# Kernel tuning notes

Hardware: AMD Instinct MI355X
Metric: run time of the kernel (lower is better)

Reference implementation:

```python
import jax, jax.numpy as jnp
import numpy as np

B = 32            # graphs in batch
NPG = 2048        # nodes per graph (equal-size graphs -> static topk sizes)
N = B * NPG
DEG = 8
E = N * DEG
IN = 64
H1 = 2 * IN       # 128
H2 = 2 * H1       # 256
K1 = NPG // 2     # SAGPooling ratio=0.5
K2 = K1 // 2
EPS = 1e-5


def _lin(k, fi, fo):
    s = 1.0 / np.sqrt(fi)
    return jax.random.uniform(k, (fi, fo), jnp.float32, -s, s)


def setup_inputs() -> dict:
    key = jax.random.key(0)
    ks = jax.random.split(key, 24)
    x = jax.random.normal(ks[0], (N, IN), jnp.float32)
    # edges strictly within each graph
    eg = jnp.repeat(jnp.arange(B, dtype=jnp.int32), NPG * DEG)
    src = eg * NPG + jax.random.randint(ks[1], (E,), 0, NPG, jnp.int32)
    tgt = eg * NPG + jax.random.randint(ks[2], (E,), 0, NPG, jnp.int32)
    edge_index = jnp.stack([src, tgt])
    batch = jnp.repeat(jnp.arange(B, dtype=jnp.int32), NPG)
    return {
        "x": x, "edge_index": edge_index, "batch": batch,
        # SAGEConv1: lin_l (neighbors, with bias) + lin_r (root, no bias)
        "W1l": _lin(ks[3], IN, H1), "b1l": jnp.zeros((H1,), jnp.float32),
        "W1r": _lin(ks[4], IN, H1),
        "bn1_g": jnp.ones((H1,), jnp.float32), "bn1_b": jnp.zeros((H1,), jnp.float32),
        # SAGPooling1 scorer = GraphConv(H1, 1): lin_rel (sum-agg, bias) + lin_root
        "p1_Wrel": _lin(ks[5], H1, 1), "p1_brel": jnp.zeros((1,), jnp.float32),
        "p1_Wroot": _lin(ks[6], H1, 1),
        "W2l": _lin(ks[7], H1, H2), "b2l": jnp.zeros((H2,), jnp.float32),
        "W2r": _lin(ks[8], H1, H2),
        "bn2_g": jnp.ones((H2,), jnp.float32), "bn2_b": jnp.zeros((H2,), jnp.float32),
        "p2_Wrel": _lin(ks[9], H2, 1), "p2_brel": jnp.zeros((1,), jnp.float32),
        "p2_Wroot": _lin(ks[10], H2, 1),
        "Wlin": _lin(ks[11], H2, 2), "blin": jnp.zeros((2,), jnp.float32),
    }


def sage_conv(x, src, tgt, emask, Wl, bl, Wr, n):
    # PyG SAGEConv: mean-aggregate x_j over valid incoming edges, then lin_l(agg)+lin_r(x)
    msg = x[src] * emask[:, None]
    s = jax.ops.segment_sum(msg, tgt, num_segments=n)
    cnt = jax.ops.segment_sum(emask, tgt, num_segments=n)
    mean = s / jnp.maximum(cnt, 1.0)[:, None]
    return mean @ Wl + bl + x @ Wr


def graph_conv_score(x, src, tgt, emask, Wrel, brel, Wroot, n):
    # PyG GraphConv (sum aggregation), out_channels=1
    s = jax.ops.segment_sum(x[src] * emask[:, None], tgt, num_segments=n)
    return (s @ Wrel + brel + x @ Wroot)[:, 0]


def batch_norm(x, g, b):
    m = x.mean(0)
    v = jnp.mean((x - m) ** 2, 0)  # biased var, as BatchNorm1d training
    return (x - m) * jax.lax.rsqrt(v + EPS) * g + b


def sag_pool(x, src, tgt, emask, score, npg, k):
    # per-graph top-k by score; x_kept scaled by tanh(score); edges re-filtered via mask
    vals, idx = jax.lax.top_k(score.reshape(B, npg), k)          # [B,k]
    perm = (jnp.arange(B, dtype=jnp.int32)[:, None] * npg + idx.astype(jnp.int32)).reshape(-1)
    xnew = x[perm] * jnp.tanh(vals.reshape(-1))[:, None]
    mapping = jnp.full((x.shape[0],), -1, jnp.int32).at[perm].set(
        jnp.arange(B * k, dtype=jnp.int32))
    ns, nt = mapping[src], mapping[tgt]
    valid = emask * ((ns >= 0) & (nt >= 0)).astype(emask.dtype)
    return xnew, jnp.maximum(ns, 0), jnp.maximum(nt, 0), valid


def reference(x, edge_index, batch, W1l, b1l, W1r, bn1_g, bn1_b,
              p1_Wrel, p1_brel, p1_Wroot, W2l, b2l, W2r, bn2_g, bn2_b,
              p2_Wrel, p2_brel, p2_Wroot, Wlin, blin):
    src, tgt = edge_index[0], edge_index[1]
    emask = jnp.ones((src.shape[0],), x.dtype)

    h = sage_conv(x, src, tgt, emask, W1l, b1l, W1r, N)
    h = jax.nn.relu(batch_norm(h, bn1_g, bn1_b))
    s1 = graph_conv_score(h, src, tgt, emask, p1_Wrel, p1_brel, p1_Wroot, N)
    h, src, tgt, emask = sag_pool(h, src, tgt, emask, s1, NPG, K1)

    n1 = B * K1
    h = sage_conv(h, src, tgt, emask, W2l, b2l, W2r, n1)
    h = jax.nn.relu(batch_norm(h, bn2_g, bn2_b))
    s2 = graph_conv_score(h, src, tgt, emask, p2_Wrel, p2_brel, p2_Wroot, n1)
    h, src, tgt, emask = sag_pool(h, src, tgt, emask, s2, K1, K2)

    batch2 = jnp.repeat(jnp.arange(B, dtype=jnp.int32), K2)
    pooled = jax.ops.segment_sum(h, batch2, num_segments=B) / jnp.asarray(K2, h.dtype)
    out = jax.nn.relu(pooled) @ Wlin + blin
    return jax.nn.softmax(out, axis=1)
```

## Files before the change

### kernel.cpp

```cpp
#include <hip/hip_runtime.h>
#include <math.h>

#define Bg   32
#define NPGc 2048
#define Nn   (Bg*NPGc)
#define DEGc 8
#define Ee   (Nn*DEGc)
#define INc  64
#define H1c  128
#define H2c  256
#define K1c  1024
#define K2c  512
#define N1c  (Bg*K1c)
#define N2c  (Bg*K2c)
#define SLAB 64

typedef __attribute__((ext_vector_type(8))) short short8;
typedef __attribute__((ext_vector_type(4))) float f32x4;

__device__ __forceinline__ ushort f2bf(float f) {
    uint u = __float_as_uint(f);
    uint r = (u + 0x7fffu + ((u >> 16) & 1u)) >> 16;
    return (ushort)r;
}
__device__ __forceinline__ float bf2f(ushort v) { return __uint_as_float((uint)v << 16); }
__device__ __forceinline__ float bfhi(uint v) { return __uint_as_float(v & 0xffff0000u); }
__device__ __forceinline__ float bflo(uint v) { return __uint_as_float(v << 16); }
__device__ __forceinline__ uint fkey(float f) {
    uint u = __float_as_uint(f);
    return u ^ ((uint)((int)u >> 31) | 0x80000000u);
}
__device__ __forceinline__ void unpk8(uint4 v, float* f) {
    f[0] = bflo(v.x); f[1] = bfhi(v.x);
    f[2] = bflo(v.y); f[3] = bfhi(v.y);
    f[4] = bflo(v.z); f[5] = bfhi(v.z);
    f[6] = bflo(v.w); f[7] = bfhi(v.w);
}
__device__ __forceinline__ uint4 pack8(const float* a, float inv) {
    uint4 o;
    o.x = (uint)f2bf(a[0] * inv) | ((uint)f2bf(a[1] * inv) << 16);
    o.y = (uint)f2bf(a[2] * inv) | ((uint)f2bf(a[3] * inv) << 16);
    o.z = (uint)f2bf(a[4] * inv) | ((uint)f2bf(a[5] * inv) << 16);
    o.w = (uint)f2bf(a[6] * inv) | ((uint)f2bf(a[7] * inv) << 16);
    return o;
}
__device__ __forceinline__ void accf8(float* a, const float* p) {
    float4 u0 = *(const float4*)p;
    float4 u1 = *(const float4*)(p + 4);
    a[0] += u0.x; a[1] += u0.y; a[2] += u0.z; a[3] += u0.w;
    a[4] += u1.x; a[5] += u1.y; a[6] += u1.z; a[7] += u1.w;
}

__global__ void init_kernel(int4* __restrict__ wc1, int4* __restrict__ dstats) {
    int id = blockIdx.x * blockDim.x + threadIdx.x;
    int4 z = {0, 0, 0, 0};
    if (id < 16384) { wc1[id] = z; return; }
    id -= 16384;
    if (id < 384)   { dstats[id] = z; }
}
#define INIT_TOTAL (16384 + 384)

__global__ void prep2_kernel(const int* __restrict__ src, const int* __restrict__ tgt,
                             const float* __restrict__ W1l, const float* __restrict__ W1r,
                             const float* __restrict__ W2l, const float* __restrict__ W2r,
                             ushort* __restrict__ T1l, ushort* __restrict__ T1r,
                             ushort* __restrict__ T2l, ushort* __restrict__ T2r,
                             int* __restrict__ wc1, int* __restrict__ col1) {
    int id = blockIdx.x * blockDim.x + threadIdx.x;
    if (id < Ee) {
        int t = tgt[id];
        int p = atomicAdd(&wc1[t], 1);
        col1[t * SLAB + p] = src[id];
        return;
    }
    id -= Ee;
    if (id < 8192) {
        int c = id / 64, k = id % 64;
        T1l[id] = f2bf(W1l[k * 128 + c]);
        T1r[id] = f2bf(W1r[k * 128 + c]);
        return;
    }
    id -= 8192;
    if (id < 32768) {
        int c = id / 128, k = id % 128;
        T2l[id] = f2bf(W2l[k * 256 + c]);
        T2r[id] = f2bf(W2r[k * 256 + c]);
    }
}
#define PREP2_TOTAL (Ee + 8192 + 32768)

__global__ __launch_bounds__(512) void gemm1f_kernel(
        const float* __restrict__ x, const int* __restrict__ deg,
        const int* __restrict__ col, const ushort* __restrict__ Wtl,
        const ushort* __restrict__ Wtr, const float* __restrict__ bias,
        ushort* __restrict__ out, double* __restrict__ dsum,
        double* __restrict__ dsq) {
    __shared__ ushort As[2][128][36];
    __shared__ ushort Bs[2][128][36];
    __shared__ float bsumS[2][128], bsqS[2][128];
    int b = blockIdx.x;
    int bs = ((b & 7) << 6) + (b >> 3);
    int m0 = bs << 7;
    int lane = threadIdx.x & 63;
    int wid = threadIdx.x >> 6;
    int wr = (wid & 1) << 6, wc = (wid >> 1) << 5;
    int l16 = lane & 15, quad = lane >> 4;

    int ar = threadIdx.x >> 2, ack = (threadIdx.x & 3) * 8;
    int anode = m0 + ar;
    int abg = anode * SLAB, adg = deg[anode];
    int4 c0h = *(const int4*)&col[abg];
    int4 c1h = *(const int4*)&col[abg + 4];
    int anb[8] = {c0h.x, c0h.y, c0h.z, c0h.w, c1h.x, c1h.y, c1h.z, c1h.w};

    f32x4 acc[4][2];
#pragma unroll
    for (int a = 0; a < 4; a++)
#pragma unroll
        for (int c = 0; c < 2; c++) acc[a][c] = (f32x4){0.f, 0.f, 0.f, 0.f};

    for (int kk0 = 0; kk0 < INc; kk0 += 32) {
        {
            int idx = threadIdx.x;
            int r = idx >> 2, ck = (idx & 3) * 8;
            *(uint4*)&Bs[0][r][ck] = *(const uint4*)&Wtl[(size_t)r * INc + kk0 + ck];
            *(uint4*)&Bs[1][r][ck] = *(const uint4*)&Wtr[(size_t)r * INc + kk0 + ck];
        }
        {
            const float* xp = &x[(size_t)anode * INc + kk0 + ack];
            float vals[8];
            float4 v0 = *(const float4*)xp, v1 = *(const float4*)(xp + 4);
            vals[0] = v0.x; vals[1] = v0.y; vals[2] = v0.z; vals[3] = v0.w;
            vals[4] = v1.x; vals[5] = v1.y; vals[6] = v1.z; vals[7] = v1.w;
            *(uint4*)&As[1][ar][ack] = pack8(vals, 1.f);
        }
        {
            float a[8] = {0.f, 0.f, 0.f, 0.f, 0.f, 0.f, 0.f, 0.f};
#pragma unroll
            for (int j = 0; j < 8; j++)
                if (j < adg) accf8(a, &x[(size_t)anb[j] * INc + kk0 + ack]);
            for (int i = abg + 8; i < abg + adg; i++)
                accf8(a, &x[(size_t)col[i] * INc + kk0 + ack]);
            int cdg = adg < 1 ? 1 : adg;
            *(uint4*)&As[0][ar][ack] = pack8(a, 1.f / (float)cdg);
        }
        __syncthreads();
        short8 a[2][4], bfr[2][2];
#pragma unroll
        for (int s = 0; s < 2; s++)
#pragma unroll
            for (int mt = 0; mt < 4; mt++)
                a[s][mt] = *(const short8*)&As[s][wr + mt * 16 + l16][quad * 8];
#pragma unroll
        for (int s = 0; s < 2; s++)
#pragma unroll
            for (int nt = 0; nt < 2; nt++)
                bfr[s][nt] = *(const short8*)&Bs[s][wc + nt * 16 + l16][quad * 8];
#pragma unroll
        for (int mt = 0; mt < 4; mt++)
#pragma unroll
            for (int nt = 0; nt < 2; nt++) {
                acc[mt][nt] = __builtin_amdgcn_mfma_f32_16x16x32_bf16(
                    a[0][mt], bfr[0][nt], acc[mt][nt], 0, 0, 0);
                acc[mt][nt] = __builtin_amdgcn_mfma_f32_16x16x32_bf16(
                    a[1][mt], bfr[1][nt], acc[mt][nt], 0, 0, 0);
            }
        __syncthreads();
    }
    float s[2] = {0.f, 0.f}, sq[2] = {0.f, 0.f};
#pragma unroll
    for (int nt = 0; nt < 2; nt++) {
        int colx = wc + nt * 16 + l16;
        float bv = bias[colx];
#pragma unroll
        for (int mt = 0; mt < 4; mt++)
#pragma unroll
            for (int rr = 0; rr < 4; rr++) {
                int row = m0 + wr + mt * 16 + quad * 4 + rr;
                float ov = acc[mt][nt][rr] + bv;
                out[(size_t)row * H1c + colx] = f2bf(ov);
                s[nt] += ov; sq[nt] += ov * ov;
            }
    }
#pragma unroll
    for (int nt = 0; nt < 2; nt++) {
        float ss = s[nt], qq = sq[nt];
        ss += __shfl_down(ss, 16); qq += __shfl_down(qq, 16);
        ss += __shfl_down(ss, 32); qq += __shfl_down(qq, 32);
        if (quad == 0) {
            bsumS[wid & 1][wc + nt * 16 + l16] = ss;
            bsqS[wid & 1][wc + nt * 16 + l16] = qq;
        }
    }
    __syncthreads();
    if (threadIdx.x < 128) {
        int c = threadIdx.x;
        atomicAdd(&dsum[c], (double)(bsumS[0][c] + bsumS[1][c]));
        atomicAdd(&dsq[c], (double)(bsqS[0][c] + bsqS[1][c]));
    }
}

template<int C>
__global__ __launch_bounds__(256) void score_kernel(const ushort* __restrict__ h,
                                                    const double* __restrict__ dsum,
                                                    const double* __restrict__ dsq,
                                                    const float* __restrict__ g,
                                                    const float* __restrict__ b,
                                                    const float* __restrict__ wrel,
                                                    const float* __restrict__ wroot,
                                                    float* __restrict__ r,
                                                    float* __restrict__ root, int n) {
    __shared__ float sc[C], sh[C], wrl[C], wrt[C];
    if ((int)threadIdx.x < C) {
        int c = threadIdx.x;
        double m = dsum[c] / (double)n;
        double var = dsq[c] / (double)n - m * m;
        float s = g[c] * (float)(1.0 / sqrt(var + 1e-5));
        sc[c] = s; sh[c] = b[c] - (float)m * s;
        wrl[c] = wrel[c]; wrt[c] = wroot[c];
    }
    __syncthreads();
    int gid = blockIdx.x * 256 + threadIdx.x;
    int node = gid >> 3, ln = gid & 7;
    float rr = 0.f, rt = 0.f;
#pragma unroll
    for (int p = 0; p < C / 64; p++) {
        int cb = p * 64 + ln * 8;
        uint4 v = *(const uint4*)&h[(size_t)node * C + cb];
        float vv[8];
        unpk8(v, vv);
#pragma unroll
        for (int q = 0; q < 8; q++) {
            int cc = cb + q;
            float val = fmaxf(vv[q] * sc[cc] + sh[cc], 0.f);
            rr += val * wrl[cc];
            rt += val * wrt[cc];
        }
    }
#pragma unroll
    for (int off = 4; off; off >>= 1) {
        rr += __shfl_down(rr, off);
        rt += __shfl_down(rt, off);
    }
    if (ln == 0) { r[node] = rr; root[node] = rt; }
}

__global__ void __launch_bounds__(1024) sel1_kernel(const float* __restrict__ r,
                                                    const float* __restrict__ root,
                                                    const int* __restrict__ deg,
                                                    const int* __restrict__ col,
                                                    const float* __restrict__ brel,
                                                    int* __restrict__ perm,
                                                    float* __restrict__ tval,
                                                    int* __restrict__ map) {
    __shared__ float rL[2048];
    __shared__ float svals[2048];
    __shared__ uint hist[257];
    __shared__ uint wsum[16];
    __shared__ uint s_b, s_rem;
    int g = blockIdx.x;
    int tid = threadIdx.x;
    int lane = tid & 63, wid = tid >> 6;
    int base = g * NPGc;
    rL[tid] = r[base + tid];
    rL[tid + 1024] = r[base + tid + 1024];
    if (tid < 257) hist[tid] = 0;
    __syncthreads();
    float bv = brel[0];
#pragma unroll
    for (int j = 0; j < 2; j++) {
        int i = tid + (j << 10);
        int node = base + i;
        float acc = bv + root[node];
        int e0 = node * SLAB, dg = deg[node];
        int4 c0 = *(const int4*)&col[e0];
        int4 c1 = *(const int4*)&col[e0 + 4];
        int nb[8] = {c0.x, c0.y, c0.z, c0.w, c1.x, c1.y, c1.z, c1.w};
#pragma unroll
        for (int q = 0; q < 8; q++)
            if (q < dg) acc += rL[nb[q] - base];
        for (int e = e0 + 8; e < e0 + dg; e++) acc += rL[col[e] - base];
        svals[i] = acc;
    }
    __syncthreads();

    uint prefix = 0, himask = 0, rem = (uint)K1c;
    for (int shift = 24; shift >= 0; shift -= 8) {
#pragma unroll
        for (int j = 0; j < 2; j++) {
            uint kk = fkey(svals[tid + (j << 10)]);
            if ((kk & himask) == prefix) atomicAdd(&hist[(kk >> shift) & 255], 1);
        }
        __syncthreads();
        if (tid < 64) {
            int L = tid;
            uint h0 = hist[4 * L], h1v = hist[4 * L + 1], h2v = hist[4 * L + 2],
                 h3 = hist[4 * L + 3];
            uint s3 = h3, s2 = h2v + s3, s1 = h1v + s2, s0 = h0 + s1;
            uint v = s0;
            for (int off = 1; off < 64; off <<= 1) {
                uint u = __shfl_down(v, off);
                if (L + off < 64) v += u;
            }
            uint above = v - s0;
            hist[4 * L] = s0 + above;
            hist[4 * L + 1] = s1 + above;
            hist[4 * L + 2] = s2 + above;
            hist[4 * L + 3] = s3 + above;
        }
        __syncthreads();
        if (tid < 256) {
            uint sb = hist[tid], sb1 = hist[tid + 1];
            if (sb >= rem && sb1 < rem) { s_b = (uint)tid; s_rem = rem - sb1; }
        }
        __syncthreads();
        prefix |= (s_b << shift);
        rem = s_rem;
        himask |= (0xFFu << shift);
        if (tid < 256) hist[tid] = 0;
        __syncthreads();
    }
    uint thr = prefix;
    uint tieM = rem;
    uint gcnt = 0, ecnt = 0, gflags = 0, eflags = 0;
#pragma unroll
    for (int j = 0; j < 2; j++) {
        uint kk = fkey(svals[tid + (j << 10)]);
        if (kk > thr) { gflags |= 1u << j; gcnt++; }
        else if (kk == thr) { eflags |= 1u << j; ecnt++; }
    }
    uint key = (gcnt << 16) | ecnt;
    uint v = key;
    for (int off = 1; off < 64; off <<= 1) {
        uint u = __shfl_up(v, off);
        if (lane >= off) v += u;
    }
    if (lane == 63) wsum[wid] = v;
    __syncthreads();
    if (tid < 16) {
        uint w0 = wsum[tid], w = w0;
        for (int off = 1; off < 16; off <<= 1) {
            uint u = __shfl_up(w, off);
            if ((int)tid >= off) w += u;
        }
        wsum[tid] = w - w0;
    }
    __syncthreads();
    uint excl = (v - key) + wsum[wid];
    uint gbase = excl >> 16, ebase = excl & 0xFFFFu;
#pragma unroll
    for (int j = 0; j < 2; j++) {
        bool gt = (gflags >> j) & 1u;
        bool eq = (eflags >> j) & 1u;
        int i = tid + (j << 10);
        int o = -1;
        if (gt || (eq && ebase < tieM)) {
            uint pos = gbase + min(ebase, tieM);
            o = g * K1c + (int)pos;
            perm[o] = base + i;
            tval[o] = tanhf(svals[i]);
        }
        map[base + i] = o;
        gbase += gt ? 1u : 0u;
        ebase += eq ? 1u : 0u;
    }
}

__global__ void __launch_bounds__(256) nofill2_kernel(
        const int* __restrict__ perm1, const int* __restrict__ map1,
        const int* __restrict__ deg1, const int* __restrict__ col1,
        int* __restrict__ wc2, int* __restrict__ col2) {
    int n = blockIdx.x * 256 + threadIdx.x;
    int o = perm1[n];
    int e0 = o * SLAB, dg = deg1[o];
    int4 c0 = *(const int4*)&col1[e0];
    int4 c1 = *(const int4*)&col1[e0 + 4];
    int nb[8] = {c0.x, c0.y, c0.z, c0.w, c1.x, c1.y, c1.z, c1.w};
    int cnt = 0;
    int ob = n * SLAB;
#pragma unroll
    for (int j = 0; j < 8; j++) {
        if (j < dg) {
            int m = map1[nb[j]];
            if (m >= 0) col2[ob + cnt++] = m;
        }
    }
    for (int e = e0 + 8; e < e0 + dg; e++) {
        int m = map1[col1[e]];
        if (m >= 0) col2[ob + cnt++] = m;
    }
    wc2[n] = cnt;
}

__global__ __launch_bounds__(512) void gemm2f_kernel(
        const ushort* __restrict__ h1, const int* __restrict__ perm1,
        const float* __restrict__ tv1, const double* __restrict__ dsum1,
        const double* __restrict__ dsq1, const float* __restrict__ bn1g,
        const float* __restrict__ bn1b, const int* __restrict__ deg,
        const int* __restrict__ col, const ushort* __restrict__ Wtl,
        const ushort* __restrict__ Wtr, const float* __restrict__ bias,
        ushort* __restrict__ out, double* __restrict__ dsum,
        double* __restrict__ dsq) {
    __shared__ ushort As[2][128][36];
    __shared__ ushort Bs[2][256][36];
    __shared__ float bsumS[2][256], bsqS[2][256];
    __shared__ float sc1[128], sh1[128];
    int b = blockIdx.x;
    int bs = ((b & 7) << 5) + (b >> 3);
    int m0 = bs << 7;
    int lane = threadIdx.x & 63;
    int wid = threadIdx.x >> 6;
    int wr = (wid & 1) << 6, wc = (wid >> 1) << 6;
    int l16 = lane & 15, quad = lane >> 4;

    if (threadIdx.x < 128) {
        int c = threadIdx.x;
        double m = dsum1[c] / (double)Nn;
        double var = dsq1[c] / (double)Nn - m * m;
        float s = bn1g[c] * (float)(1.0 / sqrt(var + 1e-5));
        sc1[c] = s; sh1[c] = bn1b[c] - (float)m * s;
    }

    int ar = threadIdx.x >> 2, ack = (threadIdx.x & 3) * 8;
    int anode = m0 + ar;
    int aold = perm1[anode];
    float atv = tv1[anode];
    int abg = anode * SLAB, adg = deg[anode];
    int4 c0h = *(const int4*)&col[abg];
    int4 c1h = *(const int4*)&col[abg + 4];
    int anb[8] = {c0h.x, c0h.y, c0h.z, c0h.w, c1h.x, c1h.y, c1h.z, c1h.w};
    int aon[8]; float atn[8];
#pragma unroll
    for (int j = 0; j < 8; j++) {
        int nbv = (j < adg) ? anb[j] : anode;
        aon[j] = perm1[nbv];
        atn[j] = tv1[nbv];
    }
    __syncthreads();

    f32x4 acc[4][4];
#pragma unroll
    for (int a = 0; a < 4; a++)
#pragma unroll
        for (int c = 0; c < 4; c++) acc[a][c] = (f32x4){0.f, 0.f, 0.f, 0.f};

    for (int kk0 = 0; kk0 < H1c; kk0 += 32) {
        for (int idx = threadIdx.x; idx < 1024; idx += 512) {
            int r = idx >> 2, ck = (idx & 3) * 8;
            *(uint4*)&Bs[0][r][ck] = *(const uint4*)&Wtl[(size_t)r * H1c + kk0 + ck];
            *(uint4*)&Bs[1][r][ck] = *(const uint4*)&Wtr[(size_t)r * H1c + kk0 + ck];
        }
        {
            uint4 hv = *(const uint4*)&h1[((size_t)aold << 7) + kk0 + ack];
            float vals[8];
            unpk8(hv, vals);
#pragma unroll
            for (int q = 0; q < 8; q++) {
                int cc = kk0 + ack + q;
                vals[q] = fmaxf(vals[q] * sc1[cc] + sh1[cc], 0.f) * atv;
            }
            *(uint4*)&As[1][ar][ack] = pack8(vals, 1.f);
        }
        {
            float a[8] = {0.f, 0.f, 0.f, 0.f, 0.f, 0.f, 0.f, 0.f};
#pragma unroll
            for (int j = 0; j < 8; j++)
                if (j < adg) {
                    uint4 u = *(const uint4*)&h1[((size_t)aon[j] << 7) + kk0 + ack];
                    float f[8];
                    unpk8(u, f);
#pragma unroll
                    for (int q = 0; q < 8; q++) {
                        int cc = kk0 + ack + q;
                        a[q] += fmaxf(f[q] * sc1[cc] + sh1[cc], 0.f) * atn[j];
                    }
                }
            for (int i = abg + 8; i < abg + adg; i++) {
                int nbv = col[i];
                int on = perm1[nbv];
                float tn = tv1[nbv];
                uint4 u = *(const uint4*)&h1[((size_t)on << 7) + kk0 + ack];
                float f[8];
                unpk8(u, f);
#pragma unroll
                for (int q = 0; q < 8; q++) {
                    int cc = kk0 + ack + q;
                    a[q] += fmaxf(f[q] * sc1[cc] + sh1[cc], 0.f) * tn;
                }
            }
            int cdg = adg < 1 ? 1 : adg;
            *(uint4*)&As[0][ar][ack] = pack8(a, 1.f / (float)cdg);
        }
        __syncthreads();
        short8 a[2][4], bfr[2][4];
#pragma unroll
        for (int s = 0; s < 2; s++)
#pragma unroll
            for (int mt = 0; mt < 4; mt++)
                a[s][mt] = *(const short8*)&As[s][wr + mt * 16 + l16][quad * 8];
#pragma unroll
        for (int s = 0; s < 2; s++)
#pragma unroll
            for (int nt = 0; nt < 4; nt++)
                bfr[s][nt] = *(const short8*)&Bs[s][wc + nt * 16 + l16][quad * 8];
#pragma unroll
        for (int mt = 0; mt < 4; mt++)
#pragma unroll
            for (int nt = 0; nt < 4; nt++) {
                acc[mt][nt] = __builtin_amdgcn_mfma_f32_16x16x32_bf16(
                    a[0][mt], bfr[0][nt], acc[mt][nt], 0, 0, 0);
                acc[mt][nt] = __builtin_amdgcn_mfma_f32_16x16x32_bf16(
                    a[1][mt], bfr[1][nt], acc[mt][nt], 0, 0, 0);
            }
        __syncthreads();
    }
    float s[4] = {0.f, 0.f, 0.f, 0.f}, sq[4] = {0.f, 0.f, 0.f, 0.f};
#pragma unroll
    for (int nt = 0; nt < 4; nt++) {
        int colx = wc + nt * 16 + l16;
        float bv = bias[colx];
#pragma unroll
        for (int mt = 0; mt < 4; mt++)
#pragma unroll
            for (int rr = 0; rr < 4; rr++) {
                int row = m0 + wr + mt * 16 + quad * 4 + rr;
                float ov = acc[mt][nt][rr] + bv;
                out[(size_t)row * H2c + colx] = f2bf(ov);
                s[nt] += ov; sq[nt] += ov * ov;
            }
    }
#pragma unroll
    for (int nt = 0; nt < 4; nt++) {
        float ss = s[nt], qq = sq[nt];
        ss += __shfl_down(ss, 16); qq += __shfl_down(qq, 16);
        ss += __shfl_down(ss, 32); qq += __shfl_down(qq, 32);
        if (quad == 0) {
            bsumS[wid & 1][wc + nt * 16 + l16] = ss;
            bsqS[wid & 1][wc + nt * 16 + l16] = qq;
        }
    }
    __syncthreads();
    if (threadIdx.x < 256) {
        int c = threadIdx.x;
        atomicAdd(&dsum[c], (double)(bsumS[0][c] + bsumS[1][c]));
        atomicAdd(&dsq[c], (double)(bsqS[0][c] + bsqS[1][c]));
    }
}

__global__ void __launch_bounds__(1024) sel2pool_kernel(
        const float* __restrict__ r, const float* __restrict__ root,
        const int* __restrict__ deg, const int* __restrict__ col,
        const float* __restrict__ brel, const ushort* __restrict__ h2,
        const double* __restrict__ dsum, const double* __restrict__ dsq,
        const float* __restrict__ g_, const float* __restrict__ b_,
        const float* __restrict__ Wlin, const float* __restrict__ blin,
        float* __restrict__ out) {
    __shared__ float rL[1024];
    __shared__ float svals[1024];
    __shared__ uint hist[257];
    __shared__ uint wsum[16];
    __shared__ uint s_b, s_rem;
    __shared__ int permL[512];
    __shared__ float tvL[512];
    __shared__ float sc[256], sh[256];
    __shared__ float part2[32][256];
    int g = blockIdx.x;
    int tid = threadIdx.x;
    int lane = tid & 63, wid = tid >> 6;
    int base = g * K1c;
    if (tid < 256) {
        int c = tid;
        double m = dsum[c] / (double)N1c;
        double var = dsq[c] / (double)N1c - m * m;
        float s = g_[c] * (float)(1.0 / sqrt(var + 1e-5));
        sc[c] = s; sh[c] = b_[c] - (float)m * s;
    }
    rL[tid] = r[base + tid];
    if (tid < 257) hist[tid] = 0;
    __syncthreads();
    {
        int node = base + tid;
        float acc = brel[0] + root[node];
        int e0 = node * SLAB, dg = deg[node];
        int4 c0 = *(const int4*)&col[e0];
        int4 c1 = *(const int4*)&col[e0 + 4];
        int nb[8] = {c0.x, c0.y, c0.z, c0.w, c1.x, c1.y, c1.z, c1.w};
#pragma unroll
        for (int q = 0; q < 8; q++)
            if (q < dg) acc += rL[nb[q] - base];
        for (int e = e0 + 8; e < e0 + dg; e++) acc += rL[col[e] - base];
        svals[tid] = acc;
    }
    __syncthreads();

    uint prefix = 0, himask = 0, rem = (uint)K2c;
    for (int shift = 24; shift >= 0; shift -= 8) {
        {
            uint kk = fkey(svals[tid]);
            if ((kk & himask) == prefix) atomicAdd(&hist[(kk >> shift) & 255], 1);
        }
        __syncthreads();
        if (tid < 64) {
            int L = tid;
            uint h0 = hist[4 * L], h1v = hist[4 * L + 1], h2v = hist[4 * L + 2],
                 h3 = hist[4 * L + 3];
            uint s3 = h3, s2 = h2v + s3, s1 = h1v + s2, s0 = h0 + s1;
            uint v = s0;
            for (int off = 1; off < 64; off <<= 1) {
                uint u = __shfl_down(v, off);
                if (L + off < 64) v += u;
            }
            uint above = v - s0;
            hist[4 * L] = s0 + above;
            hist[4 * L + 1] = s1 + above;
            hist[4 * L + 2] = s2 + above;
            hist[4 * L + 3] = s3 + above;
        }
        __syncthreads();
        if (tid < 256) {
            uint sb = hist[tid], sb1 = hist[tid + 1];
            if (sb >= rem && sb1 < rem) { s_b = (uint)tid; s_rem = rem - sb1; }
        }
        __syncthreads();
        prefix |= (s_b << shift);
        rem = s_rem;
        himask |= (0xFFu << shift);
        if (tid < 256) hist[tid] = 0;
        __syncthreads();
    }
    uint thr = prefix;
    uint tieM = rem;

    uint kk = fkey(svals[tid]);
    bool gt = kk > thr, eq = kk == thr;
    uint key = (gt ? 0x10000u : 0u) | (eq ? 1u : 0u);
    uint v = key;
    for (int off = 1; off < 64; off <<= 1) {
        uint u = __shfl_up(v, off);
        if (lane >= off) v += u;
    }
    if (lane == 63) wsum[wid] = v;
    __syncthreads();
    if (tid < 16) {
        uint w0 = wsum[tid], w = w0;
        for (int off = 1; off < 16; off <<= 1) {
            uint u = __shfl_up(w, off);
            if ((int)tid >= off) w += u;
        }
        wsum[tid] = w - w0;
    }
    __syncthreads();
    uint excl = (v - key) + wsum[wid];
    uint gbase = excl >> 16, ebase = excl & 0xFFFFu;
    if (gt || (eq && ebase < tieM)) {
        uint pos = gbase + min(ebase, tieM);
        permL[pos] = base + tid;
        tvL[pos] = tanhf(svals[tid]);
    }
    __syncthreads();

    {
        int rl = tid & 31, rg = tid >> 5;
        float a[8] = {0.f, 0.f, 0.f, 0.f, 0.f, 0.f, 0.f, 0.f};
        for (int it = 0; it < 16; it++) {
            int j = rg + it * 32;
            int row = permL[j];
            float tv = tvL[j];
            uint4 hv = *(const uint4*)&h2[((size_t)row << 8) + rl * 8];
            float f[8];
            unpk8(hv, f);
#pragma unroll
            for (int q = 0; q < 8; q++) {
                int cc = rl * 8 + q;
                a[q] += fmaxf(f[q] * sc[cc] + sh[cc], 0.f) * tv;
            }
        }
#pragma unroll
        for (int q = 0; q < 8; q++) part2[rg][rl * 8 + q] = a[q];
    }
    __syncthreads();
    if (tid < 256) {
        float s = 0.f;
#pragma unroll
        for (int gg = 0; gg < 32; gg++) s += part2[gg][tid];
        float sv = fmaxf(s * (1.f / (float)K2c), 0.f);
        rL[tid] = sv * Wlin[tid * 2 + 0];
        rL[256 + tid] = sv * Wlin[tid * 2 + 1];
    }
    __syncthreads();
    for (int off = 128; off; off >>= 1) {
        if (tid < off) { rL[tid] += rL[tid + off]; rL[256 + tid] += rL[256 + tid + off]; }
        __syncthreads();
    }
    if (tid == 0) {
        float o0 = rL[0] + blin[0], o1 = rL[256] + blin[1];
        float m = fmaxf(o0, o1);
        float e0 = expf(o0 - m), e1 = expf(o1 - m);
        float inv = 1.f / (e0 + e1);
        out[g * 2 + 0] = e0 * inv;
        out[g * 2 + 1] = e1 * inv;
    }
}

extern "C" void kernel_launch(void* const* d_in, const int* in_sizes, int n_in,
                              void* d_out, int out_size, void* d_ws, size_t ws_size,
                              hipStream_t stream) {
    const float* x      = (const float*)d_in[0];
    const int*   ei     = (const int*)d_in[1];
    const int*   src    = ei;
    const int*   tgt    = ei + Ee;
    const float* W1l    = (const float*)d_in[3];
    const float* b1l    = (const float*)d_in[4];
    const float* W1r    = (const float*)d_in[5];
    const float* bn1g   = (const float*)d_in[6];
    const float* bn1b   = (const float*)d_in[7];
    const float* p1Wrel = (const float*)d_in[8];
    const float* p1brel = (const float*)d_in[9];
    const float* p1Wroot= (const float*)d_in[10];
    const float* W2l    = (const float*)d_in[11];
    const float* b2l    = (const float*)d_in[12];
    const float* W2r    = (const float*)d_in[13];
    const float* bn2g   = (const float*)d_in[14];
    const float* bn2b   = (const float*)d_in[15];
    const float* p2Wrel = (const float*)d_in[16];
    const float* p2brel = (const float*)d_in[17];
    const float* p2Wroot= (const float*)d_in[18];
    const float* Wlin   = (const float*)d_in[19];
    const float* blin   = (const float*)d_in[20];
    float* out = (float*)d_out;
    char* ws = (char*)d_ws;

    size_t o = 0;
    auto A = [&](size_t b) { size_t r = o; o += (b + 255) & ~(size_t)255; return r; };
    size_t oH1   = A((size_t)Nn * H1c * 2);
    size_t oH2   = A((size_t)N1c * H2c * 2);
    size_t oCol1 = A((size_t)Nn * SLAB * 4);
    size_t oCol2 = A((size_t)N1c * SLAB * 4);
    size_t oWc1  = A((size_t)Nn * 4);
    size_t oR1   = A((size_t)Nn * 4);
    size_t oRoot1= A((size_t)Nn * 4);
    size_t oMap1 = A((size_t)Nn * 4);
    size_t oPerm1= A((size_t)N1c * 4);
    size_t oTv1  = A((size_t)N1c * 4);
    size_t oWc2  = A((size_t)N1c * 4);
    size_t oR2   = A((size_t)N1c * 4);
    size_t oRoot2= A((size_t)N1c * 4);
    size_t oDst  = A(768 * 8);
    size_t oWt1l = A(8192 * 2);
    size_t oWt1r = A(8192 * 2);
    size_t oWt2l = A(32768 * 2);
    size_t oWt2r = A(32768 * 2);
    (void)ws_size; (void)in_sizes; (void)n_in; (void)out_size;

    ushort* h1   = (ushort*)(ws + oH1);
    ushort* h2   = (ushort*)(ws + oH2);
    int* col1    = (int*)(ws + oCol1);
    int* col2    = (int*)(ws + oCol2);
    int* wc1     = (int*)(ws + oWc1);
    float* r1    = (float*)(ws + oR1);
    float* root1 = (float*)(ws + oRoot1);
    int* map1    = (int*)(ws + oMap1);
    int* perm1   = (int*)(ws + oPerm1);
    float* tv1   = (float*)(ws + oTv1);
    int* wc2     = (int*)(ws + oWc2);
    float* r2    = (float*)(ws + oR2);
    float* root2 = (float*)(ws + oRoot2);
    double* dsum1= (double*)(ws + oDst);
    double* dsq1 = dsum1 + 128;
    double* dsum2= dsum1 + 256;
    double* dsq2 = dsum1 + 512;
    ushort* T1l  = (ushort*)(ws + oWt1l);
    ushort* T1r  = (ushort*)(ws + oWt1r);
    ushort* T2l  = (ushort*)(ws + oWt2l);
    ushort* T2r  = (ushort*)(ws + oWt2r);

    init_kernel<<<(INIT_TOTAL + 255) / 256, 256, 0, stream>>>(
        (int4*)wc1, (int4*)dsum1);

    prep2_kernel<<<PREP2_TOTAL / 256, 256, 0, stream>>>(
        src, tgt, W1l, W1r, W2l, W2r, T1l, T1r, T2l, T2r, wc1, col1);

    gemm1f_kernel<<<512, 512, 0, stream>>>(x, wc1, col1, T1l, T1r, b1l, h1,
                                           dsum1, dsq1);

    score_kernel<H1c><<<Nn / 32, 256, 0, stream>>>(h1, dsum1, dsq1, bn1g, bn1b, p1Wrel,
                                                   p1Wroot, r1, root1, Nn);

    sel1_kernel<<<Bg, 1024, 0, stream>>>(r1, root1, wc1, col1, p1brel, perm1, tv1, map1);

    nofill2_kernel<<<N1c / 256, 256, 0, stream>>>(perm1, map1, wc1, col1, wc2, col2);

    gemm2f_kernel<<<256, 512, 0, stream>>>(h1, perm1, tv1, dsum1, dsq1, bn1g, bn1b,
                                           wc2, col2, T2l, T2r, b2l, h2, dsum2, dsq2);

    score_kernel<H2c><<<N1c / 32, 256, 0, stream>>>(h2, dsum2, dsq2, bn2g, bn2b, p2Wrel,
                                                    p2Wroot, r2, root2, N1c);

    sel2pool_kernel<<<Bg, 1024, 0, stream>>>(r2, root2, wc2, col2, p2brel, h2, dsum2,
                                             dsq2, bn2g, bn2b, Wlin, blin, out);
}
```

Before: 220.5 us.

## Gather full neighbor rows once and stage all K chunks in LDS

Both fused SAGE GEMM kernels now gather and mean-aggregate every K chunk of each neighbor row in a single pass, instead of re-walking the adjacency once per 32-wide K chunk. The aggregated A tiles for all chunks are staged in shared memory before the MFMA loop. This drops the per-chunk barriers and repeated index lookups, and raises the number of loads in flight per thread. gemm2f also double-buffers the weight tiles so the next chunk's loads overlap the current chunk's MFMAs. The cost is a much larger shared-memory footprint (about 150KB in gemm2f) and more registers, which can cut occupancy to one block per CU.

```diff
diff --git a/kernel.cpp b/kernel.cpp
--- a/kernel.cpp
+++ b/kernel.cpp
@@ -95,8 +95,8 @@
         const ushort* __restrict__ Wtr, const float* __restrict__ bias,
         ushort* __restrict__ out, double* __restrict__ dsum,
         double* __restrict__ dsq) {
-    __shared__ ushort As[2][128][36];
-    __shared__ ushort Bs[2][128][36];
+    __shared__ ushort As[2][2][128][36];
+    __shared__ ushort Bs[2][2][128][36];
     __shared__ float bsumS[2][128], bsqS[2][128];
     int b = blockIdx.x;
     int bs = ((b & 7) << 6) + (b >> 3);
@@ -113,49 +113,70 @@
     int4 c1h = *(const int4*)&col[abg + 4];
     int anb[8] = {c0h.x, c0h.y, c0h.z, c0h.w, c1h.x, c1h.y, c1h.z, c1h.w};
 
-    f32x4 acc[4][2];
-#pragma unroll
-    for (int a = 0; a < 4; a++)
-#pragma unroll
-        for (int c = 0; c < 2; c++) acc[a][c] = (f32x4){0.f, 0.f, 0.f, 0.f};
-
-    for (int kk0 = 0; kk0 < INc; kk0 += 32) {
-        {
-            int idx = threadIdx.x;
-            int r = idx >> 2, ck = (idx & 3) * 8;
-            *(uint4*)&Bs[0][r][ck] = *(const uint4*)&Wtl[(size_t)r * INc + kk0 + ck];
-            *(uint4*)&Bs[1][r][ck] = *(const uint4*)&Wtr[(size_t)r * INc + kk0 + ck];
-        }
-        {
-            const float* xp = &x[(size_t)anode * INc + kk0 + ack];
+    {
+        int r = threadIdx.x >> 2, ck = (threadIdx.x & 3) * 8;
+#pragma unroll
+        for (int kt = 0; kt < 2; kt++) {
+            *(uint4*)&Bs[0][kt][r][ck] = *(const uint4*)&Wtl[(size_t)r * INc + kt * 32 + ck];
+            *(uint4*)&Bs[1][kt][r][ck] = *(const uint4*)&Wtr[(size_t)r * INc + kt * 32 + ck];
+        }
+    }
+    {
+#pragma unroll
+        for (int kt = 0; kt < 2; kt++) {
+            const float* xp = &x[(size_t)anode * INc + kt * 32 + ack];
             float vals[8];
             float4 v0 = *(const float4*)xp, v1 = *(const float4*)(xp + 4);
             vals[0] = v0.x; vals[1] = v0.y; vals[2] = v0.z; vals[3] = v0.w;
             vals[4] = v1.x; vals[5] = v1.y; vals[6] = v1.z; vals[7] = v1.w;
-            *(uint4*)&As[1][ar][ack] = pack8(vals, 1.f);
-        }
-        {
-            float a[8] = {0.f, 0.f, 0.f, 0.f, 0.f, 0.f, 0.f, 0.f};
-#pragma unroll
-            for (int j = 0; j < 8; j++)
-                if (j < adg) accf8(a, &x[(size_t)anb[j] * INc + kk0 + ack]);
-            for (int i = abg + 8; i < abg + adg; i++)
-                accf8(a, &x[(size_t)col[i] * INc + kk0 + ack]);
-            int cdg = adg < 1 ? 1 : adg;
-            *(uint4*)&As[0][ar][ack] = pack8(a, 1.f / (float)cdg);
-        }
-        __syncthreads();
+            *(uint4*)&As[1][kt][ar][ack] = pack8(vals, 1.f);
+        }
+    }
+    {
+        float aacc[2][8];
+#pragma unroll
+        for (int kt = 0; kt < 2; kt++)
+#pragma unroll
+            for (int q = 0; q < 8; q++) aacc[kt][q] = 0.f;
+#pragma unroll
+        for (int j = 0; j < 8; j++)
+            if (j < adg) {
+                const float* xp = &x[(size_t)anb[j] * INc + ack];
+#pragma unroll
+                for (int kt = 0; kt < 2; kt++) accf8(aacc[kt], xp + kt * 32);
+            }
+        for (int i = abg + 8; i < abg + adg; i++) {
+            const float* xp = &x[(size_t)col[i] * INc + ack];
+#pragma unroll
+            for (int kt = 0; kt < 2; kt++) accf8(aacc[kt], xp + kt * 32);
+        }
+        int cdg = adg < 1 ? 1 : adg;
+        float inv = 1.f / (float)cdg;
+#pragma unroll
+        for (int kt = 0; kt < 2; kt++)
+            *(uint4*)&As[0][kt][ar][ack] = pack8(aacc[kt], inv);
+    }
+    __syncthreads();
+
+    f32x4 acc[4][2];
+#pragma unroll
+    for (int a = 0; a < 4; a++)
+#pragma unroll
+        for (int c = 0; c < 2; c++) acc[a][c] = (f32x4){0.f, 0.f, 0.f, 0.f};
+
+#pragma unroll
+    for (int kt = 0; kt < 2; kt++) {
         short8 a[2][4], bfr[2][2];
 #pragma unroll
         for (int s = 0; s < 2; s++)
 #pragma unroll
             for (int mt = 0; mt < 4; mt++)
-                a[s][mt] = *(const short8*)&As[s][wr + mt * 16 + l16][quad * 8];
+                a[s][mt] = *(const short8*)&As[s][kt][wr + mt * 16 + l16][quad * 8];
 #pragma unroll
         for (int s = 0; s < 2; s++)
 #pragma unroll
             for (int nt = 0; nt < 2; nt++)
-                bfr[s][nt] = *(const short8*)&Bs[s][wc + nt * 16 + l16][quad * 8];
+                bfr[s][nt] = *(const short8*)&Bs[s][kt][wc + nt * 16 + l16][quad * 8];
 #pragma unroll
         for (int mt = 0; mt < 4; mt++)
 #pragma unroll
@@ -165,7 +186,6 @@
                 acc[mt][nt] = __builtin_amdgcn_mfma_f32_16x16x32_bf16(
                     a[1][mt], bfr[1][nt], acc[mt][nt], 0, 0, 0);
             }
-        __syncthreads();
     }
     float s[2] = {0.f, 0.f}, sq[2] = {0.f, 0.f};
 #pragma unroll
@@ -401,8 +421,8 @@
         const ushort* __restrict__ Wtr, const float* __restrict__ bias,
         ushort* __restrict__ out, double* __restrict__ dsum,
         double* __restrict__ dsq) {
-    __shared__ ushort As[2][128][36];
-    __shared__ ushort Bs[2][256][36];
+    __shared__ ushort As[2][4][128][36];
+    __shared__ ushort Bs[2][2][256][36];
     __shared__ float bsumS[2][256], bsqS[2][256];
     __shared__ float sc1[128], sh1[128];
     int b = blockIdx.x;
@@ -438,71 +458,103 @@
     }
     __syncthreads();
 
-    f32x4 acc[4][4];
-#pragma unroll
-    for (int a = 0; a < 4; a++)
-#pragma unroll
-        for (int c = 0; c < 4; c++) acc[a][c] = (f32x4){0.f, 0.f, 0.f, 0.f};
-
-    for (int kk0 = 0; kk0 < H1c; kk0 += 32) {
-        for (int idx = threadIdx.x; idx < 1024; idx += 512) {
-            int r = idx >> 2, ck = (idx & 3) * 8;
-            *(uint4*)&Bs[0][r][ck] = *(const uint4*)&Wtl[(size_t)r * H1c + kk0 + ck];
-            *(uint4*)&Bs[1][r][ck] = *(const uint4*)&Wtr[(size_t)r * H1c + kk0 + ck];
-        }
-        {
-            uint4 hv = *(const uint4*)&h1[((size_t)aold << 7) + kk0 + ack];
+    {
+#pragma unroll
+        for (int kt = 0; kt < 4; kt++) {
+            uint4 hv = *(const uint4*)&h1[((size_t)aold << 7) + kt * 32 + ack];
             float vals[8];
             unpk8(hv, vals);
 #pragma unroll
             for (int q = 0; q < 8; q++) {
-                int cc = kk0 + ack + q;
+                int cc = kt * 32 + ack + q;
                 vals[q] = fmaxf(vals[q] * sc1[cc] + sh1[cc], 0.f) * atv;
             }
-            *(uint4*)&As[1][ar][ack] = pack8(vals, 1.f);
-        }
-        {
-            float a[8] = {0.f, 0.f, 0.f, 0.f, 0.f, 0.f, 0.f, 0.f};
-#pragma unroll
-            for (int j = 0; j < 8; j++)
-                if (j < adg) {
-                    uint4 u = *(const uint4*)&h1[((size_t)aon[j] << 7) + kk0 + ack];
+            *(uint4*)&As[1][kt][ar][ack] = pack8(vals, 1.f);
+        }
+    }
+    {
+        float aacc[4][8];
+#pragma unroll
+        for (int kt = 0; kt < 4; kt++)
+#pragma unroll
+            for (int q = 0; q < 8; q++) aacc[kt][q] = 0.f;
+#pragma unroll
+        for (int j = 0; j < 8; j++)
+            if (j < adg) {
+                const ushort* hp = &h1[(size_t)aon[j] << 7];
+                float tn = atn[j];
+#pragma unroll
+                for (int kt = 0; kt < 4; kt++) {
+                    uint4 u = *(const uint4*)&hp[kt * 32 + ack];
                     float f[8];
                     unpk8(u, f);
 #pragma unroll
                     for (int q = 0; q < 8; q++) {
-                        int cc = kk0 + ack + q;
-                        a[q] += fmaxf(f[q] * sc1[cc] + sh1[cc], 0.f) * atn[j];
+                        int cc = kt * 32 + ack + q;
+                        aacc[kt][q] += fmaxf(f[q] * sc1[cc] + sh1[cc], 0.f) * tn;
                     }
                 }
-            for (int i = abg + 8; i < abg + adg; i++) {
-                int nbv = col[i];
-                int on = perm1[nbv];
-                float tn = tv1[nbv];
-                uint4 u = *(const uint4*)&h1[((size_t)on << 7) + kk0 + ack];
+            }
+        for (int i = abg + 8; i < abg + adg; i++) {
+            int nbv = col[i];
+            int on = perm1[nbv];
+            float tn = tv1[nbv];
+            const ushort* hp = &h1[(size_t)on << 7];
+#pragma unroll
+            for (int kt = 0; kt < 4; kt++) {
+                uint4 u = *(const uint4*)&hp[kt * 32 + ack];
                 float f[8];
                 unpk8(u, f);
 #pragma unroll
                 for (int q = 0; q < 8; q++) {
-                    int cc = kk0 + ack + q;
-                    a[q] += fmaxf(f[q] * sc1[cc] + sh1[cc], 0.f) * tn;
+                    int cc = kt * 32 + ack + q;
+                    aacc[kt][q] += fmaxf(f[q] * sc1[cc] + sh1[cc], 0.f) * tn;
                 }
             }
-            int cdg = adg < 1 ? 1 : adg;
-            *(uint4*)&As[0][ar][ack] = pack8(a, 1.f / (float)cdg);
-        }
-        __syncthreads();
+        }
+        int cdg = adg < 1 ? 1 : adg;
+        float inv = 1.f / (float)cdg;
+#pragma unroll
+        for (int kt = 0; kt < 4; kt++)
+            *(uint4*)&As[0][kt][ar][ack] = pack8(aacc[kt], inv);
+    }
+    for (int idx = threadIdx.x; idx < 1024; idx += 512) {
+        int rr = idx >> 2, ck = (idx & 3) * 8;
+        *(uint4*)&Bs[0][0][rr][ck] = *(const uint4*)&Wtl[(size_t)rr * H1c + ck];
+        *(uint4*)&Bs[0][1][rr][ck] = *(const uint4*)&Wtr[(size_t)rr * H1c + ck];
+    }
+    __syncthreads();
+
+    f32x4 acc[4][4];
+#pragma unroll
+    for (int a = 0; a < 4; a++)
+#pragma unroll
+        for (int c = 0; c < 4; c++) acc[a][c] = (f32x4){0.f, 0.f, 0.f, 0.f};
+
+#pragma unroll
+    for (int kt = 0; kt < 4; kt++) {
+        int bf = kt & 1;
+        if (kt < 3) {
+            int kn = (kt + 1) * 32;
+            for (int idx = threadIdx.x; idx < 1024; idx += 512) {
+                int rr = idx >> 2, ck = (idx & 3) * 8;
+                *(uint4*)&Bs[bf ^ 1][0][rr][ck] =
+                    *(const uint4*)&Wtl[(size_t)rr * H1c + kn + ck];
+                *(uint4*)&Bs[bf ^ 1][1][rr][ck] =
+                    *(const uint4*)&Wtr[(size_t)rr * H1c + kn + ck];
+            }
+        }
         short8 a[2][4], bfr[2][4];
 #pragma unroll
         for (int s = 0; s < 2; s++)
 #pragma unroll
             for (int mt = 0; mt < 4; mt++)
-                a[s][mt] = *(const short8*)&As[s][wr + mt * 16 + l16][quad * 8];
+                a[s][mt] = *(const short8*)&As[s][kt][wr + mt * 16 + l16][quad * 8];
 #pragma unroll
         for (int s = 0; s < 2; s++)
 #pragma unroll
             for (int nt = 0; nt < 4; nt++)
-                bfr[s][nt] = *(const short8*)&Bs[s][wc + nt * 16 + l16][quad * 8];
+                bfr[s][nt] = *(const short8*)&Bs[bf][s][wc + nt * 16 + l16][quad * 8];
 #pragma unroll
         for (int mt = 0; mt < 4; mt++)
 #pragma unroll
```

Measured after the change: 218.2 us. About the same (-1.0%).
